# Kernel optimization log

Hardware: AMD Instinct MI355X
Metric: run time of the kernel (lower is better)

## Reference

```python
import jax, jax.numpy as jnp
import numpy as np

D_MODEL = 1024
N_HEADS = 16
D_HEAD = D_MODEL // N_HEADS


def setup_inputs() -> dict:
    key = jax.random.key(0)
    k1, k2, k3 = jax.random.split(key, 3)
    B, T = 2, 2048
    x = jax.random.normal(k1, (B, T, D_MODEL), dtype=jnp.float32)
    # Linear weights stored as (in, out), equivalent to torch W^T
    w_qkv = jax.random.normal(k2, (D_MODEL, 3 * D_MODEL), dtype=jnp.float32) * (D_MODEL ** -0.5)
    w_proj = jax.random.normal(k3, (D_MODEL, D_MODEL), dtype=jnp.float32) * (D_MODEL ** -0.5)
    return {"x": x, "w_qkv": w_qkv, "w_proj": w_proj}


def reference(x, w_qkv, w_proj):
    B, T, C = x.shape
    qkv = x @ w_qkv                                   # (B, T, 3C)
    qkv = qkv.reshape(B, T, 3, N_HEADS, D_HEAD)
    q, k, v = qkv[:, :, 0], qkv[:, :, 1], qkv[:, :, 2]  # (B, T, H, dh)
    q = q.transpose(0, 2, 1, 3)                        # (B, H, T, dh)
    k = k.transpose(0, 2, 1, 3)
    v = v.transpose(0, 2, 1, 3)
    scale = 1.0 / jnp.sqrt(jnp.float32(D_HEAD))
    scores = jnp.einsum('bhqd,bhkd->bhqk', q, k) * scale  # (B, H, T, T)
    causal = jnp.tril(jnp.ones((T, T), dtype=bool))
    scores = jnp.where(causal, scores, jnp.float32(-jnp.inf))
    w = jax.nn.softmax(scores, axis=-1)
    ctx = jnp.einsum('bhqk,bhkd->bhqd', w, v)          # (B, H, T, dh)
    ctx = ctx.transpose(0, 2, 1, 3).reshape(B, T, C)
    return ctx @ w_proj
```

## Files before the change

### kernel.cpp

```cpp
#include <hip/hip_runtime.h>
#include <hip/hip_bf16.h>
#include <math.h>
#include <stdint.h>

#define D_MODEL 1024
#define NHEADS  16
#define DHEAD   64
#define BATCH   2
#define SEQ     2048
#define ROWS    (BATCH*SEQ)

#define NEG_BIG (-1e30f)
#define QSCALE  0.18033688011112042f

typedef __bf16 bf16v8 __attribute__((ext_vector_type(8)));
typedef short  shortv8 __attribute__((ext_vector_type(8)));
typedef short  shortv4 __attribute__((ext_vector_type(4)));
typedef float  floatv4 __attribute__((ext_vector_type(4)));
typedef unsigned short ush;

__device__ __forceinline__ ush f2b(float f) {
  return __builtin_bit_cast(ush, (__bf16)f);
}

__device__ __forceinline__ void async16(ush* lds, const ush* g) {
  __builtin_amdgcn_global_load_lds(
      (const __attribute__((address_space(1))) void*)g,
      (__attribute__((address_space(3))) void*)lds, 16, 0, 0);
}

__global__ void detect_dtype(const uint32_t* __restrict__ x, int* __restrict__ flag) {
  if (threadIdx.x == 0 && blockIdx.x == 0) {
    int cnt = 0;
    for (int i = 0; i < 64; ++i) {
      uint32_t e = (x[i] >> 7) & 0xFF;
      cnt += (e >= 96 && e <= 144) ? 1 : 0;
    }
    *flag = (cnt >= 32) ? 1 : 0;
  }
}

__global__ __launch_bounds__(256)
void cast_to_bf16(const void* __restrict__ xin, ush* __restrict__ xb,
                  const int* __restrict__ flag) {
  int i = blockIdx.x * 256 + threadIdx.x;
  if (*flag) {
    ((shortv8*)xb)[i] = ((const shortv8*)xin)[i];
  } else {
    const floatv4* p = ((const floatv4*)xin) + (size_t)i * 2;
    floatv4 a = p[0], b = p[1];
    shortv8 o;
#pragma unroll
    for (int j = 0; j < 4; ++j) { o[j] = (short)f2b(a[j]); o[4+j] = (short)f2b(b[j]); }
    ((shortv8*)xb)[i] = o;
  }
}

__global__ __launch_bounds__(256)
void transpose_to_bf16T(const void* __restrict__ W, ush* __restrict__ Wt,
                        const int* __restrict__ flag, int K, int N) {
  __shared__ __align__(16) ush tile[64][72];
  int tiles_n = N >> 6;
  int tk = blockIdx.x / tiles_n;
  int tn = blockIdx.x % tiles_n;
  int t  = threadIdx.x;
  int r  = t >> 2;
  int c8 = (t & 3) * 8;
  int isbf = *flag;

  if (isbf) {
    const ush* src = (const ush*)W + (size_t)(tk*64 + r) * N + tn*64;
#pragma unroll
    for (int c = 0; c < 2; ++c)
      *(shortv8*)&tile[r][c8 + c*32] = *(const shortv8*)&src[c8 + c*32];
  } else {
    const float* src = (const float*)W + (size_t)(tk*64 + r) * N + tn*64;
#pragma unroll
    for (int c = 0; c < 2; ++c) {
      const floatv4* p = (const floatv4*)&src[c8 + c*32];
      floatv4 a = p[0], b = p[1];
      shortv8 o;
#pragma unroll
      for (int j = 0; j < 4; ++j) { o[j] = (short)f2b(a[j]); o[4+j] = (short)f2b(b[j]); }
      *(shortv8*)&tile[r][c8 + c*32] = o;
    }
  }
  __syncthreads();
  ush* dst = Wt + (size_t)(tn*64 + r) * K + tk*64;
#pragma unroll
  for (int c = 0; c < 2; ++c) {
    int k8 = c8 + c*32;
    shortv8 v;
#pragma unroll
    for (int j = 0; j < 8; ++j) v[j] = (short)tile[k8 + j][r];
    *(shortv8*)&dst[k8] = v;
  }
}

#define GEMM_PROLOG(Aq, Bq)                                                 \
  __shared__ __align__(16) ush smem[16384];                                 \
  const int K = 1024;                                                       \
  int bid = blockIdx.x;                                                     \
  int m0 = (bid / tiles_n) * 128;                                           \
  int n0 = (bid % tiles_n) * 128;                                           \
  int t    = threadIdx.x;                                                   \
  int lane = t & 63;                                                        \
  int w    = t >> 6;                                                        \
  int wm   = (w >> 1) * 64;                                                 \
  int wn   = (w & 1) * 64;                                                  \
  int lr   = lane & 15;                                                     \
  int quad = lane >> 4;                                                     \
  floatv4 acc[4][4] = {};                                                   \
  int r16 = lane >> 2;                                                      \
  int g4  = (lane & 3) ^ (r16 & 3);                                         \
  const ush* gA0 = Aq + (size_t)(m0 + 32*w + r16)*K + g4*8;                 \
  const ush* gA1 = gA0 + (size_t)16*K;                                      \
  const ush* gB0 = Bq + (size_t)(n0 + 32*w + r16)*K + g4*8;                 \
  const ush* gB1 = gB0 + (size_t)16*K;                                      \
  int fs = (quad ^ (lr & 3)) * 8;                                           \
  async16(&smem[(32*w)*32], gA0);                                           \
  async16(&smem[(32*w+16)*32], gA1);                                        \
  async16(&smem[8192 + (32*w)*32], gB0);                                    \
  async16(&smem[8192 + (32*w+16)*32], gB1);                                 \
  for (int kk = 0; kk < K; kk += 32) {                                      \
    int cur = (kk >> 5) & 1;                                                \
    __syncthreads();                                                        \
    if (kk + 32 < K) {                                                      \
      int nx = cur ^ 1;                                                     \
      async16(&smem[nx*4096 + (32*w)*32], gA0 + kk + 32);                   \
      async16(&smem[nx*4096 + (32*w+16)*32], gA1 + kk + 32);                \
      async16(&smem[8192 + nx*4096 + (32*w)*32], gB0 + kk + 32);            \
      async16(&smem[8192 + nx*4096 + (32*w+16)*32], gB1 + kk + 32);         \
    }                                                                       \
    bf16v8 af[4], bfr[4];                                                   \
    _Pragma("unroll")                                                       \
    for (int i = 0; i < 4; ++i) {                                           \
      af[i]  = *(bf16v8*)&smem[cur*4096 + (wm + i*16 + lr)*32 + fs];        \
      bfr[i] = *(bf16v8*)&smem[8192 + cur*4096 + (wn + i*16 + lr)*32 + fs]; \
    }                                                                       \
    _Pragma("unroll")                                                       \
    for (int i = 0; i < 4; ++i)                                             \
      _Pragma("unroll")                                                     \
      for (int j = 0; j < 4; ++j)                                           \
        acc[i][j] = __builtin_amdgcn_mfma_f32_16x16x32_bf16(bfr[i], af[j],  \
                                                            acc[i][j], 0, 0, 0); \
  }

__global__ __launch_bounds__(256, 3)
void gemm_qkv(const ush* __restrict__ A, const ush* __restrict__ Bt,
              ush* __restrict__ qb_, ush* __restrict__ kb_, ush* __restrict__ vb_,
              int tiles_n) {
  GEMM_PROLOG(A, Bt)

  int nwb = n0 + wn;
  int s   = nwb >> 10;
  int h   = (nwb & 1023) >> 6;
  int b   = (m0 + wm) >> 11;
  int bh  = b*16 + h;
  int ttw = (m0 + wm) & 2047;

  __syncthreads();

  if (s < 2) {
    ush* dst = (s == 0) ? qb_ : kb_;
    float sc = (s == 0) ? QSCALE : 1.0f;
#pragma unroll
    for (int i = 0; i < 4; ++i) {
      int d4 = i*16 + quad*4;
#pragma unroll
      for (int j = 0; j < 4; ++j) {
        int tt = ttw + j*16 + lr;
        shortv4 v4;
#pragma unroll
        for (int r = 0; r < 4; ++r) v4[r] = (short)f2b(acc[i][j][r] * sc);
        *(shortv4*)&dst[((size_t)bh*SEQ + tt)*64 + d4] = v4;
      }
    }
  } else {
    ush* L = &smem[w*4096];
#pragma unroll
    for (int i = 0; i < 4; ++i) {
#pragma unroll
      for (int r = 0; r < 4; ++r) {
        int dl = i*16 + quad*4 + r;
        shortv4 p4;
#pragma unroll
        for (int j = 0; j < 4; ++j) p4[j] = (short)f2b(acc[i][j][r]);
        int slot = (lr >> 1) ^ (dl & 7);
        *(shortv4*)&L[dl*64 + slot*8 + (lr & 1)*4] = p4;
      }
    }
#pragma unroll
    for (int p = 0; p < 8; ++p) {
      int dl = p*8 + (lane >> 3);
      int c8 = lane & 7;
      int slot = c8 ^ (dl & 7);
      shortv8 v = *(shortv8*)&L[dl*64 + slot*8];
      *(shortv8*)&vb_[((size_t)bh*64 + dl)*SEQ + ttw + c8*8] = v;
    }
  }
}

__global__ __launch_bounds__(256, 4)
void gemm_bt(const ush* __restrict__ A, const ush* __restrict__ Bt,
             void* __restrict__ Cp, const int* __restrict__ flag,
             int ldc, int tiles_n) {
  __shared__ __align__(16) ush smem[12288];
  const int K = 1024;
  int bid = blockIdx.x;
  int m0 = (bid / tiles_n) * 64;
  int n0 = (bid % tiles_n) * 128;
  int t    = threadIdx.x;
  int lane = t & 63;
  int w    = t >> 6;
  int wm   = (w >> 1) * 32;
  int wn   = (w & 1) * 64;
  int lr   = lane & 15;
  int quad = lane >> 4;
  floatv4 acc[4][2] = {};
  int r16 = lane >> 2;
  int g4  = (lane & 3) ^ (r16 & 3);
  const ush* gA0 = A  + (size_t)(m0 + 16*w + r16)*K + g4*8;
  const ush* gB0 = Bt + (size_t)(n0 + 32*w + r16)*K + g4*8;
  const ush* gB1 = gB0 + (size_t)16*K;
  int fs = (quad ^ (lr & 3)) * 8;

  async16(&smem[(16*w)*32], gA0);
  async16(&smem[4096 + (32*w)*32], gB0);
  async16(&smem[4096 + (32*w+16)*32], gB1);

  for (int kk = 0; kk < K; kk += 32) {
    int cur = (kk >> 5) & 1;
    __syncthreads();
    if (kk + 32 < K) {
      int nx = cur ^ 1;
      async16(&smem[nx*2048 + (16*w)*32], gA0 + kk + 32);
      async16(&smem[4096 + nx*4096 + (32*w)*32], gB0 + kk + 32);
      async16(&smem[4096 + nx*4096 + (32*w+16)*32], gB1 + kk + 32);
    }
    bf16v8 af[2], bfr[4];
#pragma unroll
    for (int j = 0; j < 2; ++j)
      af[j] = *(bf16v8*)&smem[cur*2048 + (wm + j*16 + lr)*32 + fs];
#pragma unroll
    for (int i = 0; i < 4; ++i)
      bfr[i] = *(bf16v8*)&smem[4096 + cur*4096 + (wn + i*16 + lr)*32 + fs];
#pragma unroll
    for (int i = 0; i < 4; ++i)
#pragma unroll
      for (int j = 0; j < 2; ++j)
        acc[i][j] = __builtin_amdgcn_mfma_f32_16x16x32_bf16(bfr[i], af[j],
                                                            acc[i][j], 0, 0, 0);
  }

  int f32out = (flag != nullptr) && (*flag == 0);
  if (f32out) {
    float* Cf = (float*)Cp;
#pragma unroll
    for (int i = 0; i < 4; ++i) {
      int nb = n0 + wn + i*16 + quad*4;
#pragma unroll
      for (int j = 0; j < 2; ++j) {
        int row = m0 + wm + j*16 + lr;
        *(floatv4*)&Cf[(size_t)row*ldc + nb] = acc[i][j];
      }
    }
  } else {
    __hip_bfloat16* Cb = (__hip_bfloat16*)Cp;
#pragma unroll
    for (int i = 0; i < 4; ++i) {
      int nb = n0 + wn + i*16 + quad*4;
#pragma unroll
      for (int j = 0; j < 2; ++j) {
        int row = m0 + wm + j*16 + lr;
        shortv4 v4;
#pragma unroll
        for (int r = 0; r < 4; ++r) v4[r] = (short)f2b(acc[i][j][r]);
        *(shortv4*)&((ush*)Cb)[(size_t)row*ldc + nb] = v4;
      }
    }
  }
}

#define PSTR 72
#define MFMA16(a,b,c) __builtin_amdgcn_mfma_f32_16x16x32_bf16(a,b,c,0,0,0)

__device__ __forceinline__ void softpack(const floatv4* s, int qw, int kb0,
                                         bool diag, ush* PsW, int quad, int lr) {
  if (diag) {
#pragma unroll
    for (int r = 0; r < 4; ++r) {
      int qv = qw + quad*4 + r;
      shortv4 p4;
#pragma unroll
      for (int j = 0; j < 4; ++j) {
        float z = (kb0 + 16*j + lr > qv) ? NEG_BIG : s[j][r];
        p4[j] = (short)f2b(__builtin_amdgcn_exp2f(z));
      }
      *(shortv4*)&PsW[(quad*4 + r)*PSTR + lr*4] = p4;
    }
  } else {
#pragma unroll
    for (int r = 0; r < 4; ++r) {
      shortv4 p4;
#pragma unroll
      for (int j = 0; j < 4; ++j)
        p4[j] = (short)f2b(__builtin_amdgcn_exp2f(s[j][r]));
      *(shortv4*)&PsW[(quad*4 + r)*PSTR + lr*4] = p4;
    }
  }
}

__global__ __launch_bounds__(256, 4)
void attn_fwd(const ush* __restrict__ qb_, const ush* __restrict__ kb_,
              const ush* __restrict__ vb_, __hip_bfloat16* __restrict__ ctx) {
  __shared__ __align__(16) ush Ks[2][64*64];
  __shared__ __align__(16) ush Vt[2][64*64];
  __shared__ __align__(16) ush Ps[2][4][16*PSTR];

  int bid = blockIdx.x;
  int p   = bid & 15;
  int h   = (bid >> 4) & 15;
  int b   = bid >> 8;
  int bh  = b*16 + h;

  int t = threadIdx.x, w = t >> 6, lane = t & 63, lr = lane & 15, quad = lane >> 4;

  const ush* qh = qb_ + (size_t)bh * SEQ * 64;
  const ush* kh = kb_ + (size_t)bh * SEQ * 64;
  const ush* vh = vb_ + (size_t)bh * 64 * SEQ;

  int qA = p, qB = 31 - p;
  int qwA = qA*64 + w*16, qwB = qB*64 + w*16;

  const ush* qpA = qh + (size_t)(qwA + lr)*64;
  bf16v8 qfA0 = *(const bf16v8*)&qpA[quad*8];
  bf16v8 qfA1 = *(const bf16v8*)&qpA[32 + quad*8];
  const ush* qpB = qh + (size_t)(qwB + lr)*64;
  bf16v8 qfB0 = *(const bf16v8*)&qpB[quad*8];
  bf16v8 qfB1 = *(const bf16v8*)&qpB[32 + quad*8];

  floatv4 accA[4] = {}, accB[4] = {}, aclA = {}, aclB = {};

  bf16v8 ones;
#pragma unroll
  for (int j = 0; j < 8; ++j) ones[j] = (__bf16)1.0f;

  int r8 = lane >> 3;
  int s8 = lane & 7;
  int g8 = s8 ^ r8;
  const ush* kg0 = kh + (size_t)(16*w     + r8)*64 + g8*8;
  const ush* kg1 = kh + (size_t)(16*w + 8 + r8)*64 + g8*8;
  const ush* vg0 = vh + (size_t)(16*w     + r8)*SEQ + g8*8;
  const ush* vg1 = vh + (size_t)(16*w + 8 + r8)*SEQ + g8*8;
  int lo0 = (16*w)*64, lo1 = (16*w + 8)*64;

  int sl0 = quad ^ (lr & 7);
  int sl1 = (quad + 4) ^ (lr & 7);

  int ntiles = 32 - p;

  async16(&Ks[0][lo0], kg0);
  async16(&Ks[0][lo1], kg1);
  async16(&Vt[0][lo0], vg0);
  async16(&Vt[0][lo1], vg1);

  for (int tk = 0; tk < ntiles; ++tk) {
    int cur = tk & 1;
    __syncthreads();
    if (tk + 1 < ntiles) {
      int nx = cur ^ 1;
      size_t ko = (size_t)(tk + 1) * 64 * 64;
      size_t vo = (size_t)(tk + 1) * 64;
      async16(&Ks[nx][lo0], kg0 + ko);
      async16(&Ks[nx][lo1], kg1 + ko);
      async16(&Vt[nx][lo0], vg0 + vo);
      async16(&Vt[nx][lo1], vg1 + vo);
    }

    int kb0 = tk * 64;
    bool liveA = (tk <= p);
    bool diagA = (tk == p);
    bool diagB = (tk == qB);

    floatv4 sA[4] = {}, sB[4] = {};
#pragma unroll
    for (int j = 0; j < 4; ++j) {
      bool mA = liveA && (!diagA || j <= w);
      bool mB = (!diagB || j <= w);
      if (mA | mB) {
        int row = 16*j + lr;
        bf16v8 kf0 = *(bf16v8*)&Ks[cur][row*64 + sl0*8];
        bf16v8 kf1 = *(bf16v8*)&Ks[cur][row*64 + sl1*8];
        if (mA) { sA[j] = MFMA16(qfA0, kf0, sA[j]); sA[j] = MFMA16(qfA1, kf1, sA[j]); }
        if (mB) { sB[j] = MFMA16(qfB0, kf0, sB[j]); sB[j] = MFMA16(qfB1, kf1, sB[j]); }
      }
    }

    if (liveA) softpack(sA, qwA, kb0, diagA, &Ps[0][w][0], quad, lr);
    softpack(sB, qwB, kb0, diagB, &Ps[1][w][0], quad, lr);

    bf16v8 pfA0, pfA1;
    if (liveA) {
      pfA0 = *(bf16v8*)&Ps[0][w][lr*PSTR + quad*8];
      pfA1 = *(bf16v8*)&Ps[0][w][lr*PSTR + 32 + quad*8];
      aclA = MFMA16(pfA0, ones, aclA);
      aclA = MFMA16(pfA1, ones, aclA);
    }
    bf16v8 pfB0 = *(bf16v8*)&Ps[1][w][lr*PSTR + quad*8];
    bf16v8 pfB1 = *(bf16v8*)&Ps[1][w][lr*PSTR + 32 + quad*8];
    aclB = MFMA16(pfB0, ones, aclB);
    aclB = MFMA16(pfB1, ones, aclB);

#pragma unroll
    for (int c = 0; c < 4; ++c) {
      int row = 16*c + lr;
      bf16v8 vf0 = *(bf16v8*)&Vt[cur][row*64 + sl0*8];
      bf16v8 vf1 = *(bf16v8*)&Vt[cur][row*64 + sl1*8];
      if (liveA) { accA[c] = MFMA16(pfA0, vf0, accA[c]); accA[c] = MFMA16(pfA1, vf1, accA[c]); }
      accB[c] = MFMA16(pfB0, vf0, accB[c]);
      accB[c] = MFMA16(pfB1, vf1, accB[c]);
    }
  }

#pragma unroll
  for (int r = 0; r < 4; ++r) {
    float invA = 1.0f / fmaxf(aclA[r], 1e-30f);
    float invB = 1.0f / fmaxf(aclB[r], 1e-30f);
    size_t oA = (size_t)(b*SEQ + qwA + quad*4 + r) * D_MODEL + h*64;
    size_t oB = (size_t)(b*SEQ + qwB + quad*4 + r) * D_MODEL + h*64;
#pragma unroll
    for (int c = 0; c < 4; ++c) {
      ctx[oA + c*16 + lr] = __float2bfloat16(accA[c][r] * invA);
      ctx[oB + c*16 + lr] = __float2bfloat16(accB[c][r] * invB);
    }
  }
}

extern "C" void kernel_launch(void* const* d_in, const int* in_sizes, int n_in,
                              void* d_out, int out_size, void* d_ws, size_t ws_size,
                              hipStream_t stream) {
  const void* x      = d_in[0];
  const void* w_qkv  = d_in[1];
  const void* w_proj = d_in[2];

  int* flag   = (int*)d_ws;
  ush* xb     = (ush*)d_ws + 8;
  ush* wqkvT  = xb     + (size_t)ROWS * D_MODEL;
  ush* wprojT = wqkvT  + (size_t)3072 * 1024;
  ush* qbuf   = wprojT + (size_t)1024 * 1024;
  ush* kbuf   = qbuf   + (size_t)32 * SEQ * 64;
  ush* vbuf   = kbuf   + (size_t)32 * SEQ * 64;
  ush* ctx    = xb;

  detect_dtype<<<1, 64, 0, stream>>>((const uint32_t*)x, flag);

  cast_to_bf16<<<(ROWS*D_MODEL/8)/256, 256, 0, stream>>>(x, xb, flag);

  transpose_to_bf16T<<<(1024/64)*(3072/64), 256, 0, stream>>>(w_qkv,  wqkvT, flag, 1024, 3072);
  transpose_to_bf16T<<<(1024/64)*(1024/64), 256, 0, stream>>>(w_proj, wprojT, flag, 1024, 1024);

  gemm_qkv<<<(ROWS/128)*(3072/128), 256, 0, stream>>>(
      xb, wqkvT, qbuf, kbuf, vbuf, 3072/128);

  attn_fwd<<<BATCH * NHEADS * 16, 256, 0, stream>>>(
      qbuf, kbuf, vbuf, (__hip_bfloat16*)ctx);

  gemm_bt<<<(ROWS/64)*(1024/128), 256, 0, stream>>>(
      ctx, wprojT, d_out, flag, 1024, 1024/128);
}
```

Baseline: 205.3 us.

## Split paired query tiles across two warp groups in 512-thread attention blocks

The attention kernel goes from 256 to 512 threads per block. Each group of four wavefronts now handles one of the two paired query tiles (p and 31-p), where before every wavefront computed both tiles. Each wavefront now loads half as many K/V rows per tile and holds half as many accumulators, which cuts register pressure and raises wave-level parallelism. The cost is that the A-group waves sit idle after tile p while the B group continues, so waves are load-imbalanced and the whole block waits at each barrier.

```diff
diff --git a/kernel.cpp b/kernel.cpp
--- a/kernel.cpp
+++ b/kernel.cpp
@@ -311,12 +311,12 @@
   }
 }
 
-__global__ __launch_bounds__(256, 4)
+__global__ __launch_bounds__(512, 4)
 void attn_fwd(const ush* __restrict__ qb_, const ush* __restrict__ kb_,
               const ush* __restrict__ vb_, __hip_bfloat16* __restrict__ ctx) {
   __shared__ __align__(16) ush Ks[2][64*64];
   __shared__ __align__(16) ush Vt[2][64*64];
-  __shared__ __align__(16) ush Ps[2][4][16*PSTR];
+  __shared__ __align__(16) ush Ps[8][16*PSTR];
 
   int bid = blockIdx.x;
   int p   = bid & 15;
@@ -324,23 +324,22 @@
   int b   = bid >> 8;
   int bh  = b*16 + h;
 
-  int t = threadIdx.x, w = t >> 6, lane = t & 63, lr = lane & 15, quad = lane >> 4;
+  int t = threadIdx.x, w8 = t >> 6, lane = t & 63, lr = lane & 15, quad = lane >> 4;
+  int isB = w8 >> 2;
+  int w   = w8 & 3;
 
   const ush* qh = qb_ + (size_t)bh * SEQ * 64;
   const ush* kh = kb_ + (size_t)bh * SEQ * 64;
   const ush* vh = vb_ + (size_t)bh * 64 * SEQ;
 
-  int qA = p, qB = 31 - p;
-  int qwA = qA*64 + w*16, qwB = qB*64 + w*16;
-
-  const ush* qpA = qh + (size_t)(qwA + lr)*64;
-  bf16v8 qfA0 = *(const bf16v8*)&qpA[quad*8];
-  bf16v8 qfA1 = *(const bf16v8*)&qpA[32 + quad*8];
-  const ush* qpB = qh + (size_t)(qwB + lr)*64;
-  bf16v8 qfB0 = *(const bf16v8*)&qpB[quad*8];
-  bf16v8 qfB1 = *(const bf16v8*)&qpB[32 + quad*8];
-
-  floatv4 accA[4] = {}, accB[4] = {}, aclA = {}, aclB = {};
+  int qt = isB ? (31 - p) : p;
+  int qw = qt*64 + w*16;
+
+  const ush* qp = qh + (size_t)(qw + lr)*64;
+  bf16v8 qf0 = *(const bf16v8*)&qp[quad*8];
+  bf16v8 qf1 = *(const bf16v8*)&qp[32 + quad*8];
+
+  floatv4 acc[4] = {}, acl = {};
 
   bf16v8 ones;
 #pragma unroll
@@ -349,91 +348,69 @@
   int r8 = lane >> 3;
   int s8 = lane & 7;
   int g8 = s8 ^ r8;
-  const ush* kg0 = kh + (size_t)(16*w     + r8)*64 + g8*8;
-  const ush* kg1 = kh + (size_t)(16*w + 8 + r8)*64 + g8*8;
-  const ush* vg0 = vh + (size_t)(16*w     + r8)*SEQ + g8*8;
-  const ush* vg1 = vh + (size_t)(16*w + 8 + r8)*SEQ + g8*8;
-  int lo0 = (16*w)*64, lo1 = (16*w + 8)*64;
+  const ush* kg = kh + (size_t)(8*w8 + r8)*64 + g8*8;
+  const ush* vg = vh + (size_t)(8*w8 + r8)*SEQ + g8*8;
+  int lo = (8*w8)*64;
 
   int sl0 = quad ^ (lr & 7);
   int sl1 = (quad + 4) ^ (lr & 7);
 
   int ntiles = 32 - p;
 
-  async16(&Ks[0][lo0], kg0);
-  async16(&Ks[0][lo1], kg1);
-  async16(&Vt[0][lo0], vg0);
-  async16(&Vt[0][lo1], vg1);
+  async16(&Ks[0][lo], kg);
+  async16(&Vt[0][lo], vg);
 
   for (int tk = 0; tk < ntiles; ++tk) {
     int cur = tk & 1;
     __syncthreads();
     if (tk + 1 < ntiles) {
       int nx = cur ^ 1;
-      size_t ko = (size_t)(tk + 1) * 64 * 64;
-      size_t vo = (size_t)(tk + 1) * 64;
-      async16(&Ks[nx][lo0], kg0 + ko);
-      async16(&Ks[nx][lo1], kg1 + ko);
-      async16(&Vt[nx][lo0], vg0 + vo);
-      async16(&Vt[nx][lo1], vg1 + vo);
-    }
-
-    int kb0 = tk * 64;
-    bool liveA = (tk <= p);
-    bool diagA = (tk == p);
-    bool diagB = (tk == qB);
-
-    floatv4 sA[4] = {}, sB[4] = {};
-#pragma unroll
-    for (int j = 0; j < 4; ++j) {
-      bool mA = liveA && (!diagA || j <= w);
-      bool mB = (!diagB || j <= w);
-      if (mA | mB) {
-        int row = 16*j + lr;
-        bf16v8 kf0 = *(bf16v8*)&Ks[cur][row*64 + sl0*8];
-        bf16v8 kf1 = *(bf16v8*)&Ks[cur][row*64 + sl1*8];
-        if (mA) { sA[j] = MFMA16(qfA0, kf0, sA[j]); sA[j] = MFMA16(qfA1, kf1, sA[j]); }
-        if (mB) { sB[j] = MFMA16(qfB0, kf0, sB[j]); sB[j] = MFMA16(qfB1, kf1, sB[j]); }
-      }
-    }
-
-    if (liveA) softpack(sA, qwA, kb0, diagA, &Ps[0][w][0], quad, lr);
-    softpack(sB, qwB, kb0, diagB, &Ps[1][w][0], quad, lr);
-
-    bf16v8 pfA0, pfA1;
-    if (liveA) {
-      pfA0 = *(bf16v8*)&Ps[0][w][lr*PSTR + quad*8];
-      pfA1 = *(bf16v8*)&Ps[0][w][lr*PSTR + 32 + quad*8];
-      aclA = MFMA16(pfA0, ones, aclA);
-      aclA = MFMA16(pfA1, ones, aclA);
-    }
-    bf16v8 pfB0 = *(bf16v8*)&Ps[1][w][lr*PSTR + quad*8];
-    bf16v8 pfB1 = *(bf16v8*)&Ps[1][w][lr*PSTR + 32 + quad*8];
-    aclB = MFMA16(pfB0, ones, aclB);
-    aclB = MFMA16(pfB1, ones, aclB);
-
-#pragma unroll
-    for (int c = 0; c < 4; ++c) {
-      int row = 16*c + lr;
-      bf16v8 vf0 = *(bf16v8*)&Vt[cur][row*64 + sl0*8];
-      bf16v8 vf1 = *(bf16v8*)&Vt[cur][row*64 + sl1*8];
-      if (liveA) { accA[c] = MFMA16(pfA0, vf0, accA[c]); accA[c] = MFMA16(pfA1, vf1, accA[c]); }
-      accB[c] = MFMA16(pfB0, vf0, accB[c]);
-      accB[c] = MFMA16(pfB1, vf1, accB[c]);
+      async16(&Ks[nx][lo], kg + (size_t)(tk + 1) * 64 * 64);
+      async16(&Vt[nx][lo], vg + (size_t)(tk + 1) * 64);
+    }
+
+    bool live = isB | (tk <= p);
+    if (live) {
+      int kb0 = tk * 64;
+      bool diag = (tk == qt);
+
+      floatv4 s[4] = {};
+#pragma unroll
+      for (int j = 0; j < 4; ++j) {
+        if (!diag || j <= w) {
+          int row = 16*j + lr;
+          bf16v8 kf0 = *(bf16v8*)&Ks[cur][row*64 + sl0*8];
+          bf16v8 kf1 = *(bf16v8*)&Ks[cur][row*64 + sl1*8];
+          s[j] = MFMA16(qf0, kf0, s[j]);
+          s[j] = MFMA16(qf1, kf1, s[j]);
+        }
+      }
+
+      softpack(s, qw, kb0, diag, &Ps[w8][0], quad, lr);
+
+      bf16v8 pf0 = *(bf16v8*)&Ps[w8][lr*PSTR + quad*8];
+      bf16v8 pf1 = *(bf16v8*)&Ps[w8][lr*PSTR + 32 + quad*8];
+      acl = MFMA16(pf0, ones, acl);
+      acl = MFMA16(pf1, ones, acl);
+
+#pragma unroll
+      for (int c = 0; c < 4; ++c) {
+        int row = 16*c + lr;
+        bf16v8 vf0 = *(bf16v8*)&Vt[cur][row*64 + sl0*8];
+        bf16v8 vf1 = *(bf16v8*)&Vt[cur][row*64 + sl1*8];
+        acc[c] = MFMA16(pf0, vf0, acc[c]);
+        acc[c] = MFMA16(pf1, vf1, acc[c]);
+      }
     }
   }
 
 #pragma unroll
   for (int r = 0; r < 4; ++r) {
-    float invA = 1.0f / fmaxf(aclA[r], 1e-30f);
-    float invB = 1.0f / fmaxf(aclB[r], 1e-30f);
-    size_t oA = (size_t)(b*SEQ + qwA + quad*4 + r) * D_MODEL + h*64;
-    size_t oB = (size_t)(b*SEQ + qwB + quad*4 + r) * D_MODEL + h*64;
-#pragma unroll
-    for (int c = 0; c < 4; ++c) {
-      ctx[oA + c*16 + lr] = __float2bfloat16(accA[c][r] * invA);
-      ctx[oB + c*16 + lr] = __float2bfloat16(accB[c][r] * invB);
-    }
+    float inv = 1.0f / fmaxf(acl[r], 1e-30f);
+    size_t o = (size_t)(b*SEQ + qw + quad*4 + r) * D_MODEL + h*64;
+#pragma unroll
+    for (int c = 0; c < 4; ++c)
+      ctx[o + c*16 + lr] = __float2bfloat16(acc[c][r] * inv);
   }
 }
 
@@ -463,7 +440,7 @@
   gemm_qkv<<<(ROWS/128)*(3072/128), 256, 0, stream>>>(
       xb, wqkvT, qbuf, kbuf, vbuf, 3072/128);
 
-  attn_fwd<<<BATCH * NHEADS * 16, 256, 0, stream>>>(
+  attn_fwd<<<BATCH * NHEADS * 16, 512, 0, stream>>>(
       qbuf, kbuf, vbuf, (__hip_bfloat16*)ctx);
 
   gemm_bt<<<(ROWS/64)*(1024/128), 256, 0, stream>>>(
```

Result: faster. 195.8 us (-4.6%).
